# Kernel optimization log

Measured on AMD Instinct MI355X. Metric: run time of the kernel, lower is better.

## Reference

```python
import jax, jax.numpy as jnp
import numpy as np

N = 50000
E = 1_600_000
N_INP = 128
N_HID = 128
N_OUT = 64
N_LAYERS = 2


def setup_inputs() -> dict:
    key = jax.random.key(0)
    ks = jax.random.split(key, 12)
    s = 1.0 / np.sqrt(N_HID)
    return {
        "node_attr": jax.random.normal(ks[0], (N, N_INP), dtype=jnp.float32),
        "edge_index": jax.random.randint(ks[1], (2, E), 0, N, dtype=jnp.int64),
        "batch_idx": jnp.zeros((N,), dtype=jnp.int64),
        "adv_atts": jax.random.uniform(ks[2], (N_LAYERS, E), dtype=jnp.float32, minval=0.05, maxval=1.0),
        "W_inp": jax.random.normal(ks[3], (N_HID, N_INP), dtype=jnp.float32) * (1.0 / np.sqrt(N_INP)),
        "b_inp": jnp.zeros((N_HID,), dtype=jnp.float32),
        "W_a": jax.random.normal(ks[4], (N_LAYERS, N_HID, N_HID), dtype=jnp.float32) * s,
        "b_a": jnp.zeros((N_LAYERS, N_HID), dtype=jnp.float32),
        "ln_w": jnp.ones((N_LAYERS, N_HID), dtype=jnp.float32),
        "ln_b": jnp.zeros((N_LAYERS, N_HID), dtype=jnp.float32),
        "W_out": jax.random.normal(ks[5], (N_OUT, N_HID), dtype=jnp.float32) * s,
        "b_out": jnp.zeros((N_OUT,), dtype=jnp.float32),
    }


def _layer_norm(x, w, b, eps=1e-5):
    mu = jnp.mean(x, axis=-1, keepdims=True)
    var = jnp.mean(jnp.square(x - mu), axis=-1, keepdims=True)
    return (x - mu) * jax.lax.rsqrt(var + eps) * w + b


def _segment_softmax(logits, seg, num_segments):
    # PyG softmax: numerically-stable softmax grouped by target node id
    m = jax.ops.segment_max(logits, seg, num_segments=num_segments)
    e = jnp.exp(logits - m[seg])
    s = jax.ops.segment_sum(e, seg, num_segments=num_segments)
    return e / (s[seg] + 1e-16)


def reference(node_attr, edge_index, batch_idx, adv_atts,
              W_inp, b_inp, W_a, b_a, ln_w, ln_b, W_out, b_out):
    src = edge_index[0]  # j (source)
    dst = edge_index[1]  # i (target)
    n = node_attr.shape[0]
    # dropout is identity at inference; initial norm is overwritten (dead code)
    node_rep = node_attr @ W_inp.T + b_inp  # [N, H]
    for l in range(W_a.shape[0]):
        att = _segment_softmax(jnp.log(adv_atts[l]), dst, n)        # [E]
        msg = node_rep[src] * att[:, None]                          # [E, H]
        aggr = jax.ops.segment_sum(msg, dst, num_segments=n)        # [N, H]
        h = (aggr + node_rep) @ W_a[l].T + b_a[l]
        node_rep = _layer_norm(jax.nn.gelu(h, approximate=False), ln_w[l], ln_b[l])
    # node_level == True
    return node_rep @ W_out.T + b_out
```

## Files before the change

### kernel.cpp

```cpp
#include <hip/hip_runtime.h>
#include <hip/hip_bf16.h>
#include <math.h>


#define WAVE 64
#define NPARTS 32
#define CHUNKE 4096
#define CB 64

typedef __attribute__((ext_vector_type(8))) short bf16x8;
typedef __attribute__((ext_vector_type(4))) float f32x4;
union ABu { uint4 u; bf16x8 v; };
union ABh { ushort h[8]; bf16x8 v; };

static __device__ __forceinline__ float bf2f(uint u16) {
    union { uint i; float f; } c;
    c.i = u16 << 16;
    return c.f;
}
static __device__ __forceinline__ uint f2bf(float f) {
    uint x = __float_as_uint(f);
    return (x + 0x7FFFu + ((x >> 16) & 1u)) >> 16;
}

__global__ __launch_bounds__(512) void k_bin(const int* __restrict__ src,
                                             const int* __restrict__ dst,
                                             const float* __restrict__ adv,
                                             int E, int PART,
                                             int* __restrict__ deg,
                                             int4* __restrict__ tmp,
                                             int* __restrict__ bstart,
                                             int* __restrict__ bcnt) {
    __shared__ int hist[NPARTS], cur[NPARTS], base_[NPARTS];
    __shared__ int4 buf[CHUNKE];
    int c = blockIdx.x;
    int e0 = c * CHUNKE;
    int cnt = min(CHUNKE, E - e0);
    int dreg[CHUNKE / 512];
    int preg[CHUNKE / 512];
    if (threadIdx.x < NPARTS) hist[threadIdx.x] = 0;
    __syncthreads();
#pragma unroll
    for (int i = 0; i < CHUNKE / 512; ++i) {
        int idx = threadIdx.x + i * 512;
        if (idx < cnt) {
            int d = dst[e0 + idx];
            int pt = d / PART;
            dreg[i] = d;
            preg[i] = pt;
            atomicAdd(&hist[pt], 1);
        }
    }
    __syncthreads();
    if (threadIdx.x < 64) {
        int t = threadIdx.x;
        int v = (t < NPARTS) ? hist[t] : 0;
#pragma unroll
        for (int off = 1; off < NPARTS; off <<= 1) {
            int u = __shfl_up(v, off);
            if (t >= off) v += u;
        }
        if (t < NPARTS) {
            base_[t] = v - hist[t];
            cur[t] = v - hist[t];
        }
    }
    __syncthreads();
#pragma unroll
    for (int i = 0; i < CHUNKE / 512; ++i) {
        int idx = threadIdx.x + i * 512;
        if (idx < cnt) {
            int e = e0 + idx;
            int slot = atomicAdd(&cur[preg[i]], 1);
            int rk = atomicAdd(&deg[dreg[i]], 1);
            buf[slot] = make_int4(src[e], __float_as_int(adv[e]),
                                  __float_as_int(adv[E + e]),
                                  dreg[i] | (rk << 16));
        }
    }
    __syncthreads();
    for (int i = threadIdx.x; i < cnt; i += 512) tmp[(size_t)e0 + i] = buf[i];
    if (threadIdx.x < NPARTS) {
        bstart[c * NPARTS + threadIdx.x] = e0 + base_[threadIdx.x];
        bcnt[c * NPARTS + threadIdx.x] = hist[threadIdx.x];
    }
}

__global__ __launch_bounds__(256) void k_scan1(const int* __restrict__ deg, int n,
                                               int* __restrict__ excl,
                                               int* __restrict__ bsum) {
    __shared__ int sd[256];
    int t = threadIdx.x, i = blockIdx.x * 256 + t;
    int v = (i < n) ? deg[i] : 0;
    sd[t] = v;
    __syncthreads();
    for (int off = 1; off < 256; off <<= 1) {
        int u = (t >= off) ? sd[t - off] : 0;
        __syncthreads();
        sd[t] += u;
        __syncthreads();
    }
    if (i < n) excl[i] = sd[t] - v;
    if (t == 255) bsum[blockIdx.x] = sd[255];
}

__global__ __launch_bounds__(256) void k_scan3b(const int* __restrict__ deg,
                                                const int* __restrict__ excl,
                                                const int* __restrict__ bsum,
                                                int nbs, int n,
                                                int* __restrict__ row_ptr) {
    __shared__ int sd[256];
    int t = threadIdx.x;
    int v = (t < nbs) ? bsum[t] : 0;
    sd[t] = v;
    __syncthreads();
    for (int off = 1; off < 256; off <<= 1) {
        int u = (t >= off) ? sd[t - off] : 0;
        __syncthreads();
        sd[t] += u;
        __syncthreads();
    }
    int pref = (blockIdx.x == 0) ? 0 : sd[blockIdx.x - 1];
    int i = blockIdx.x * 256 + t;
    if (i < n) {
        int rp = pref + excl[i];
        row_ptr[i] = rp;
        if (i == n - 1) row_ptr[n] = rp + deg[i];
    }
}

__global__ __launch_bounds__(256) void k_place(const int4* __restrict__ tmp,
                                               const int* __restrict__ bstart,
                                               const int* __restrict__ bcnt,
                                               const int* __restrict__ row_ptr,
                                               int nchunk,
                                               int2* __restrict__ csr0,
                                               int2* __restrict__ csr1) {
    int xcd = blockIdx.x & 7;
    int j = blockIdx.x >> 3;
    for (int ph = 0; ph < NPARTS / 8; ++ph) {
        int part = xcd + 8 * ph;
        for (int c = j; c < nchunk; c += CB) {
            int s = bstart[c * NPARTS + part];
            int cnt = bcnt[c * NPARTS + part];
            for (int i = threadIdx.x; i < cnt; i += 256) {
                int4 r = tmp[(size_t)s + i];
                int d = r.w & 0xffff;
                int rk = ((uint)r.w) >> 16;
                int pos = row_ptr[d] + rk;
                csr0[pos] = make_int2(r.x, r.y);
                csr1[pos] = make_int2(r.x, r.z);
            }
        }
    }
}

__global__ __launch_bounds__(512) void k_aggr(const uint* __restrict__ rep32,
                                              const int* __restrict__ row_ptr,
                                              const int2* __restrict__ csr,
                                              uint* __restrict__ xout, int n) {
    int wave = threadIdx.x >> 6, lane = threadIdx.x & 63;
    int node = blockIdx.x * 8 + wave;
    if (node >= n) return;
    int s0 = row_ptr[node], s1 = row_ptr[node + 1];
    float accx = 0.f, accy = 0.f, ssum = 0.f, amax = 0.f;
    int s = s0;
    for (; s + 16 <= s1; s += 16) {
        int2 cc[16];
        uint rr[16];
#pragma unroll
        for (int k = 0; k < 16; ++k) cc[k] = csr[s + k];
#pragma unroll
        for (int k = 0; k < 16; ++k) rr[k] = rep32[(size_t)cc[k].x * 64 + lane];
#pragma unroll
        for (int k = 0; k < 16; ++k) {
            float a = __int_as_float(cc[k].y);
            ssum += a;
            amax = fmaxf(amax, a);
            accx = fmaf(a, bf2f(rr[k] & 0xffffu), accx);
            accy = fmaf(a, bf2f(rr[k] >> 16), accy);
        }
    }
    for (; s + 4 <= s1; s += 4) {
        int2 cc[4];
        uint rr[4];
#pragma unroll
        for (int k = 0; k < 4; ++k) cc[k] = csr[s + k];
#pragma unroll
        for (int k = 0; k < 4; ++k) rr[k] = rep32[(size_t)cc[k].x * 64 + lane];
#pragma unroll
        for (int k = 0; k < 4; ++k) {
            float a = __int_as_float(cc[k].y);
            ssum += a;
            amax = fmaxf(amax, a);
            accx = fmaf(a, bf2f(rr[k] & 0xffffu), accx);
            accy = fmaf(a, bf2f(rr[k] >> 16), accy);
        }
    }
    for (; s < s1; ++s) {
        int2 c = csr[s];
        float a = __int_as_float(c.y);
        uint r = rep32[(size_t)c.x * 64 + lane];
        ssum += a;
        amax = fmaxf(amax, a);
        accx = fmaf(a, bf2f(r & 0xffffu), accx);
        accy = fmaf(a, bf2f(r >> 16), accy);
    }
    float inv = (s1 > s0) ? 1.f / (ssum + amax * 1e-16f) : 0.f;
    uint m = rep32[(size_t)node * 64 + lane];
    float ox = fmaf(accx, inv, bf2f(m & 0xffffu));
    float oy = fmaf(accy, inv, bf2f(m >> 16));
    xout[(size_t)node * 64 + lane] = f2bf(ox) | (f2bf(oy) << 16);
}

#define WROW 136

__global__ __launch_bounds__(512) void k_mlp(const uint* __restrict__ x32,
                                             const float* __restrict__ W,
                                             const float* __restrict__ b,
                                             const float* __restrict__ lw,
                                             const float* __restrict__ lb,
                                             uint* __restrict__ out32, int n) {
    __shared__ ushort Wbf[128 * WROW];
    uint* wd = (uint*)Wbf;
    for (int idx = threadIdx.x; idx < 128 * 64; idx += 512) {
        int row = idx >> 6, d = idx & 63;
        float2 w2 = *(const float2*)&W[row * 128 + d * 2];
        wd[row * (WROW / 2) + d] = f2bf(w2.x) | (f2bf(w2.y) << 16);
    }
    __syncthreads();
    int wv = threadIdx.x >> 6, l = threadIdx.x & 63;
    int c = l & 15, q = l >> 4;
    int base = blockIdx.x * 256 + wv * 32;
    int r0 = min(base + c, n - 1);
    int r1 = min(base + 16 + c, n - 1);

    f32x4 acc[2][8];
#pragma unroll
    for (int rt = 0; rt < 2; ++rt)
#pragma unroll
        for (int ct = 0; ct < 8; ++ct) acc[rt][ct] = (f32x4){0.f, 0.f, 0.f, 0.f};

#pragma unroll
    for (int kb = 0; kb < 4; ++kb) {
        ABu a0, a1;
        a0.u = *(const uint4*)&x32[(size_t)r0 * 64 + kb * 16 + q * 4];
        a1.u = *(const uint4*)&x32[(size_t)r1 * 64 + kb * 16 + q * 4];
#pragma unroll
        for (int ct = 0; ct < 8; ++ct) {
            bf16x8 bf = *(const bf16x8*)&Wbf[(ct * 16 + c) * WROW + kb * 32 + q * 8];
            acc[0][ct] = __builtin_amdgcn_mfma_f32_16x16x32_bf16(a0.v, bf, acc[0][ct], 0, 0, 0);
            acc[1][ct] = __builtin_amdgcn_mfma_f32_16x16x32_bf16(a1.v, bf, acc[1][ct], 0, 0, 0);
        }
    }

    float bias[8], lwv[8], lbv[8];
#pragma unroll
    for (int ct = 0; ct < 8; ++ct) {
        bias[ct] = b[ct * 16 + c];
        lwv[ct] = lw[ct * 16 + c];
        lbv[ct] = lb[ct * 16 + c];
    }

#pragma unroll
    for (int rt = 0; rt < 2; ++rt) {
#pragma unroll
        for (int ct = 0; ct < 8; ++ct)
#pragma unroll
            for (int i = 0; i < 4; ++i) {
                float h = acc[rt][ct][i] + bias[ct];
                acc[rt][ct][i] = 0.5f * h * (1.f + erff(h * 0.70710678118654752f));
            }
        float mu[4], rstd[4];
#pragma unroll
        for (int i = 0; i < 4; ++i) {
            float s = 0.f;
#pragma unroll
            for (int ct = 0; ct < 8; ++ct) s += acc[rt][ct][i];
            s += __shfl_xor(s, 1);
            s += __shfl_xor(s, 2);
            s += __shfl_xor(s, 4);
            s += __shfl_xor(s, 8);
            mu[i] = s * (1.f / 128.f);
        }
#pragma unroll
        for (int i = 0; i < 4; ++i) {
            float v = 0.f;
#pragma unroll
            for (int ct = 0; ct < 8; ++ct) {
                float d = acc[rt][ct][i] - mu[i];
                v += d * d;
            }
            v += __shfl_xor(v, 1);
            v += __shfl_xor(v, 2);
            v += __shfl_xor(v, 4);
            v += __shfl_xor(v, 8);
            rstd[i] = rsqrtf(v * (1.f / 128.f) + 1e-5f);
        }
#pragma unroll
        for (int ct = 0; ct < 8; ++ct)
#pragma unroll
            for (int i = 0; i < 4; ++i) {
                float o = (acc[rt][ct][i] - mu[i]) * rstd[i] * lwv[ct] + lbv[ct];
                float p = __shfl_xor(o, 1);
                uint dw = (c & 1) ? (f2bf(p) | (f2bf(o) << 16))
                                  : (f2bf(o) | (f2bf(p) << 16));
                int R = base + rt * 16 + q * 4 + i;
                if (R < n && (c & 1) == 0)
                    out32[(size_t)R * 64 + ct * 8 + (c >> 1)] = dw;
            }
    }
}

__global__ __launch_bounds__(512) void k_input(const float* __restrict__ attr,
                                               const float* __restrict__ W,
                                               const float* __restrict__ b,
                                               uint* __restrict__ out32, int n) {
    __shared__ ushort Wbf[128 * WROW];
    uint* wd = (uint*)Wbf;
    for (int idx = threadIdx.x; idx < 128 * 64; idx += 512) {
        int row = idx >> 6, d = idx & 63;
        float2 w2 = *(const float2*)&W[row * 128 + d * 2];
        wd[row * (WROW / 2) + d] = f2bf(w2.x) | (f2bf(w2.y) << 16);
    }
    __syncthreads();
    int wv = threadIdx.x >> 6, l = threadIdx.x & 63;
    int c = l & 15, q = l >> 4;
    int base = blockIdx.x * 256 + wv * 32;
    int r0 = min(base + c, n - 1);
    int r1 = min(base + 16 + c, n - 1);

    f32x4 acc[2][8];
#pragma unroll
    for (int rt = 0; rt < 2; ++rt)
#pragma unroll
        for (int ct = 0; ct < 8; ++ct) acc[rt][ct] = (f32x4){0.f, 0.f, 0.f, 0.f};

#pragma unroll
    for (int kb = 0; kb < 4; ++kb) {
        ABh a0, a1;
        float4 f0 = *(const float4*)&attr[(size_t)r0 * 128 + kb * 32 + q * 8];
        float4 f1 = *(const float4*)&attr[(size_t)r0 * 128 + kb * 32 + q * 8 + 4];
        a0.h[0] = f2bf(f0.x); a0.h[1] = f2bf(f0.y); a0.h[2] = f2bf(f0.z); a0.h[3] = f2bf(f0.w);
        a0.h[4] = f2bf(f1.x); a0.h[5] = f2bf(f1.y); a0.h[6] = f2bf(f1.z); a0.h[7] = f2bf(f1.w);
        float4 g0 = *(const float4*)&attr[(size_t)r1 * 128 + kb * 32 + q * 8];
        float4 g1 = *(const float4*)&attr[(size_t)r1 * 128 + kb * 32 + q * 8 + 4];
        a1.h[0] = f2bf(g0.x); a1.h[1] = f2bf(g0.y); a1.h[2] = f2bf(g0.z); a1.h[3] = f2bf(g0.w);
        a1.h[4] = f2bf(g1.x); a1.h[5] = f2bf(g1.y); a1.h[6] = f2bf(g1.z); a1.h[7] = f2bf(g1.w);
#pragma unroll
        for (int ct = 0; ct < 8; ++ct) {
            bf16x8 bf = *(const bf16x8*)&Wbf[(ct * 16 + c) * WROW + kb * 32 + q * 8];
            acc[0][ct] = __builtin_amdgcn_mfma_f32_16x16x32_bf16(a0.v, bf, acc[0][ct], 0, 0, 0);
            acc[1][ct] = __builtin_amdgcn_mfma_f32_16x16x32_bf16(a1.v, bf, acc[1][ct], 0, 0, 0);
        }
    }
    float bias[8];
#pragma unroll
    for (int ct = 0; ct < 8; ++ct) bias[ct] = b[ct * 16 + c];
#pragma unroll
    for (int rt = 0; rt < 2; ++rt)
#pragma unroll
        for (int ct = 0; ct < 8; ++ct)
#pragma unroll
            for (int i = 0; i < 4; ++i) {
                float o = acc[rt][ct][i] + bias[ct];
                float p = __shfl_xor(o, 1);
                uint dw = (c & 1) ? (f2bf(p) | (f2bf(o) << 16))
                                  : (f2bf(o) | (f2bf(p) << 16));
                int R = base + rt * 16 + q * 4 + i;
                if (R < n && (c & 1) == 0)
                    out32[(size_t)R * 64 + ct * 8 + (c >> 1)] = dw;
            }
}

__global__ __launch_bounds__(512) void k_out(const uint* __restrict__ rep32,
                                             const float* __restrict__ W,
                                             const float* __restrict__ b,
                                             float* __restrict__ out, int n) {
    __shared__ ushort Wbf[64 * WROW];
    uint* wd = (uint*)Wbf;
    for (int idx = threadIdx.x; idx < 64 * 64; idx += 512) {
        int row = idx >> 6, d = idx & 63;
        float2 w2 = *(const float2*)&W[row * 128 + d * 2];
        wd[row * (WROW / 2) + d] = f2bf(w2.x) | (f2bf(w2.y) << 16);
    }
    __syncthreads();
    int wv = threadIdx.x >> 6, l = threadIdx.x & 63;
    int c = l & 15, q = l >> 4;
    int base = blockIdx.x * 256 + wv * 32;
    int r0 = min(base + c, n - 1);
    int r1 = min(base + 16 + c, n - 1);

    f32x4 acc[2][4];
#pragma unroll
    for (int rt = 0; rt < 2; ++rt)
#pragma unroll
        for (int ct = 0; ct < 4; ++ct) acc[rt][ct] = (f32x4){0.f, 0.f, 0.f, 0.f};

#pragma unroll
    for (int kb = 0; kb < 4; ++kb) {
        ABu a0, a1;
        a0.u = *(const uint4*)&rep32[(size_t)r0 * 64 + kb * 16 + q * 4];
        a1.u = *(const uint4*)&rep32[(size_t)r1 * 64 + kb * 16 + q * 4];
#pragma unroll
        for (int ct = 0; ct < 4; ++ct) {
            bf16x8 bf = *(const bf16x8*)&Wbf[(ct * 16 + c) * WROW + kb * 32 + q * 8];
            acc[0][ct] = __builtin_amdgcn_mfma_f32_16x16x32_bf16(a0.v, bf, acc[0][ct], 0, 0, 0);
            acc[1][ct] = __builtin_amdgcn_mfma_f32_16x16x32_bf16(a1.v, bf, acc[1][ct], 0, 0, 0);
        }
    }
    float bias[4];
#pragma unroll
    for (int ct = 0; ct < 4; ++ct) bias[ct] = b[ct * 16 + c];
#pragma unroll
    for (int rt = 0; rt < 2; ++rt)
#pragma unroll
        for (int ct = 0; ct < 4; ++ct)
#pragma unroll
            for (int i = 0; i < 4; ++i) {
                int R = base + rt * 16 + q * 4 + i;
                if (R < n) out[(size_t)R * 64 + ct * 16 + c] = acc[rt][ct][i] + bias[ct];
            }
}

extern "C" void kernel_launch(void* const* d_in, const int* in_sizes, int n_in,
                              void* d_out, int out_size, void* d_ws, size_t ws_size,
                              hipStream_t stream) {
    const float* node_attr = (const float*)d_in[0];
    const int* ei = (const int*)d_in[1];
    const float* adv = (const float*)d_in[3];
    const float* W_inp = (const float*)d_in[4];
    const float* b_inp = (const float*)d_in[5];
    const float* W_a = (const float*)d_in[6];
    const float* b_a = (const float*)d_in[7];
    const float* ln_w = (const float*)d_in[8];
    const float* ln_b = (const float*)d_in[9];
    const float* W_out = (const float*)d_in[10];
    const float* b_out = (const float*)d_in[11];

    const int n = in_sizes[0] / 128;
    const int E = in_sizes[1] / 2;
    const int nchunk = (E + CHUNKE - 1) / CHUNKE;
    const int PART = (n + NPARTS - 1) / NPARTS;

    int2* csr0 = (int2*)d_ws;
    int2* csr1 = csr0 + E;
    int4* tmp = (int4*)(csr1 + E);
    uint* A = (uint*)tmp;
    uint* B = A + (size_t)n * 64;
    int* deg = (int*)(tmp + E);
    int* excl = deg + n;
    int* row_ptr = excl + n;
    int* bsum = row_ptr + n + 1;
    int* bstart = bsum + 256;
    int* bcnt = bstart + (size_t)nchunk * NPARTS;

    const int* src = ei;
    const int* dst = ei + E;

    hipMemsetAsync(deg, 0, (size_t)n * sizeof(int), stream);

    int nbs = (n + 255) / 256;
    k_bin<<<nchunk, 512, 0, stream>>>(src, dst, adv, E, PART, deg, tmp, bstart, bcnt);
    k_scan1<<<nbs, 256, 0, stream>>>(deg, n, excl, bsum);
    k_scan3b<<<nbs, 256, 0, stream>>>(deg, excl, bsum, nbs, n, row_ptr);
    k_place<<<8 * CB, 256, 0, stream>>>(tmp, bstart, bcnt, row_ptr, nchunk, csr0, csr1);

    int nbd = (n + 255) / 256;
    int nb8 = (n + 7) / 8;
    k_input<<<nbd, 512, 0, stream>>>(node_attr, W_inp, b_inp, A, n);

    k_aggr<<<nb8, 512, 0, stream>>>(A, row_ptr, csr0, B, n);
    k_mlp<<<nbd, 512, 0, stream>>>(B, W_a, b_a, ln_w, ln_b, A, n);
    k_aggr<<<nb8, 512, 0, stream>>>(A, row_ptr, csr1, B, n);
    k_mlp<<<nbd, 512, 0, stream>>>(B, W_a + 128 * 128, b_a + 128,
                                   ln_w + 128, ln_b + 128, A, n);

    k_out<<<nbd, 512, 0, stream>>>(A, W_out, b_out, (float*)d_out, n);
}
```

Before: 305.4 us.

## Replace global degree atomics with per-partition LDS histograms for CSR build

The CSR construction no longer does a global atomicAdd on per-node degree counters inside the binning kernel. A new k_deg kernel instead builds per-partition, per-chunk-range histograms in shared memory. The scans then derive row pointers plus per-range base offsets from these, and k_place assigns positions with LDS atomics. This removes contended global atomics and the memset, at the cost of an extra pass over the binned records and a nondeterministic within-row edge order.

Result: faster. 278.8 us (-8.7%).

```diff
diff --git a/kernel.cpp b/kernel.cpp
--- a/kernel.cpp
+++ b/kernel.cpp
@@ -6,7 +6,7 @@
 #define WAVE 64
 #define NPARTS 32
 #define CHUNKE 4096
-#define CB 64
+#define PARTMAX 2048
 
 typedef __attribute__((ext_vector_type(8))) short bf16x8;
 typedef __attribute__((ext_vector_type(4))) float f32x4;
@@ -27,7 +27,6 @@
                                              const int* __restrict__ dst,
                                              const float* __restrict__ adv,
                                              int E, int PART,
-                                             int* __restrict__ deg,
                                              int4* __restrict__ tmp,
                                              int* __restrict__ bstart,
                                              int* __restrict__ bcnt) {
@@ -72,10 +71,8 @@
         if (idx < cnt) {
             int e = e0 + idx;
             int slot = atomicAdd(&cur[preg[i]], 1);
-            int rk = atomicAdd(&deg[dreg[i]], 1);
             buf[slot] = make_int4(src[e], __float_as_int(adv[e]),
-                                  __float_as_int(adv[E + e]),
-                                  dreg[i] | (rk << 16));
+                                  __float_as_int(adv[E + e]), dreg[i]);
         }
     }
     __syncthreads();
@@ -86,12 +83,40 @@
     }
 }
 
-__global__ __launch_bounds__(256) void k_scan1(const int* __restrict__ deg, int n,
+__global__ __launch_bounds__(256) void k_deg(const int4* __restrict__ tmp,
+                                             const int* __restrict__ bstart,
+                                             const int* __restrict__ bcnt,
+                                             int nchunk, int crange, int PART, int n,
+                                             int* __restrict__ histg) {
+    __shared__ int h[PARTMAX];
+    int part = blockIdx.x & 31, r = blockIdx.x >> 5;
+    for (int j = threadIdx.x; j < PART; j += 256) h[j] = 0;
+    __syncthreads();
+    int c0 = r * crange, c1 = min(c0 + crange, nchunk);
+    int lo = part * PART;
+    for (int c = c0; c < c1; ++c) {
+        int s = bstart[c * NPARTS + part];
+        int cnt = bcnt[c * NPARTS + part];
+        for (int i = threadIdx.x; i < cnt; i += 256)
+            atomicAdd(&h[tmp[(size_t)s + i].w - lo], 1);
+    }
+    __syncthreads();
+    for (int j = threadIdx.x; j < PART; j += 256)
+        histg[(size_t)(part * 8 + r) * PART + j] = h[j];
+}
+
+__global__ __launch_bounds__(256) void k_scan1(const int* __restrict__ histg,
+                                               int PART, int n,
                                                int* __restrict__ excl,
                                                int* __restrict__ bsum) {
     __shared__ int sd[256];
     int t = threadIdx.x, i = blockIdx.x * 256 + t;
-    int v = (i < n) ? deg[i] : 0;
+    int v = 0;
+    if (i < n) {
+        int part = i / PART, off = i - part * PART;
+#pragma unroll
+        for (int r = 0; r < 8; ++r) v += histg[(size_t)(part * 8 + r) * PART + off];
+    }
     sd[t] = v;
     __syncthreads();
     for (int off = 1; off < 256; off <<= 1) {
@@ -104,10 +129,10 @@
     if (t == 255) bsum[blockIdx.x] = sd[255];
 }
 
-__global__ __launch_bounds__(256) void k_scan3b(const int* __restrict__ deg,
+__global__ __launch_bounds__(256) void k_scan3b(int* __restrict__ histg,
                                                 const int* __restrict__ excl,
                                                 const int* __restrict__ bsum,
-                                                int nbs, int n,
+                                                int nbs, int n, int PART,
                                                 int* __restrict__ row_ptr) {
     __shared__ int sd[256];
     int t = threadIdx.x;
@@ -125,32 +150,41 @@
     if (i < n) {
         int rp = pref + excl[i];
         row_ptr[i] = rp;
-        if (i == n - 1) row_ptr[n] = rp + deg[i];
+        int part = i / PART, off = i - part * PART;
+        int run = rp;
+#pragma unroll
+        for (int r = 0; r < 8; ++r) {
+            size_t idx = (size_t)(part * 8 + r) * PART + off;
+            int h = histg[idx];
+            histg[idx] = run;
+            run += h;
+        }
+        if (i == n - 1) row_ptr[n] = run;
     }
 }
 
 __global__ __launch_bounds__(256) void k_place(const int4* __restrict__ tmp,
                                                const int* __restrict__ bstart,
                                                const int* __restrict__ bcnt,
-                                               const int* __restrict__ row_ptr,
-                                               int nchunk,
+                                               const int* __restrict__ rbase,
+                                               int nchunk, int crange, int PART, int n,
                                                int2* __restrict__ csr0,
                                                int2* __restrict__ csr1) {
-    int xcd = blockIdx.x & 7;
-    int j = blockIdx.x >> 3;
-    for (int ph = 0; ph < NPARTS / 8; ++ph) {
-        int part = xcd + 8 * ph;
-        for (int c = j; c < nchunk; c += CB) {
-            int s = bstart[c * NPARTS + part];
-            int cnt = bcnt[c * NPARTS + part];
-            for (int i = threadIdx.x; i < cnt; i += 256) {
-                int4 r = tmp[(size_t)s + i];
-                int d = r.w & 0xffff;
-                int rk = ((uint)r.w) >> 16;
-                int pos = row_ptr[d] + rk;
-                csr0[pos] = make_int2(r.x, r.y);
-                csr1[pos] = make_int2(r.x, r.z);
-            }
+    __shared__ int cur[PARTMAX];
+    int part = blockIdx.x & 31, r = blockIdx.x >> 5;
+    for (int j = threadIdx.x; j < PART; j += 256)
+        cur[j] = rbase[(size_t)(part * 8 + r) * PART + j];
+    __syncthreads();
+    int c0 = r * crange, c1 = min(c0 + crange, nchunk);
+    int lo = part * PART;
+    for (int c = c0; c < c1; ++c) {
+        int s = bstart[c * NPARTS + part];
+        int cnt = bcnt[c * NPARTS + part];
+        for (int i = threadIdx.x; i < cnt; i += 256) {
+            int4 rec = tmp[(size_t)s + i];
+            int pos = atomicAdd(&cur[rec.w - lo], 1);
+            csr0[pos] = make_int2(rec.x, rec.y);
+            csr1[pos] = make_int2(rec.x, rec.z);
         }
     }
 }
@@ -442,14 +476,15 @@
     const int E = in_sizes[1] / 2;
     const int nchunk = (E + CHUNKE - 1) / CHUNKE;
     const int PART = (n + NPARTS - 1) / NPARTS;
+    const int crange = (nchunk + 7) / 8;
 
     int2* csr0 = (int2*)d_ws;
     int2* csr1 = csr0 + E;
     int4* tmp = (int4*)(csr1 + E);
     uint* A = (uint*)tmp;
     uint* B = A + (size_t)n * 64;
-    int* deg = (int*)(tmp + E);
-    int* excl = deg + n;
+    int* histg = (int*)(tmp + E);
+    int* excl = histg + (size_t)NPARTS * 8 * PART;
     int* row_ptr = excl + n;
     int* bsum = row_ptr + n + 1;
     int* bstart = bsum + 256;
@@ -458,13 +493,13 @@
     const int* src = ei;
     const int* dst = ei + E;
 
-    hipMemsetAsync(deg, 0, (size_t)n * sizeof(int), stream);
-
     int nbs = (n + 255) / 256;
-    k_bin<<<nchunk, 512, 0, stream>>>(src, dst, adv, E, PART, deg, tmp, bstart, bcnt);
-    k_scan1<<<nbs, 256, 0, stream>>>(deg, n, excl, bsum);
-    k_scan3b<<<nbs, 256, 0, stream>>>(deg, excl, bsum, nbs, n, row_ptr);
-    k_place<<<8 * CB, 256, 0, stream>>>(tmp, bstart, bcnt, row_ptr, nchunk, csr0, csr1);
+    k_bin<<<nchunk, 512, 0, stream>>>(src, dst, adv, E, PART, tmp, bstart, bcnt);
+    k_deg<<<256, 256, 0, stream>>>(tmp, bstart, bcnt, nchunk, crange, PART, n, histg);
+    k_scan1<<<nbs, 256, 0, stream>>>(histg, PART, n, excl, bsum);
+    k_scan3b<<<nbs, 256, 0, stream>>>(histg, excl, bsum, nbs, n, PART, row_ptr);
+    k_place<<<256, 256, 0, stream>>>(tmp, bstart, bcnt, histg, nchunk, crange,
+                                     PART, n, csr0, csr1);
 
     int nbd = (n + 255) / 256;
     int nb8 = (n + 7) / 8;
```
